# Kernel optimization log

Hardware: AMD Instinct MI355X
Metric: run time of the kernel (lower is better)

The kernel has to match this reference:

```python
import jax, jax.numpy as jnp
import numpy as np

IN_F, OUT_F = 512, 512
GRID_SIZE, SPLINE_ORDER = 5, 3
K = GRID_SIZE + SPLINE_ORDER  # 8 basis functions
B, S = 8, 1024


def setup_inputs() -> dict:
    key = jax.random.key(0)
    k1, k2, k3, k4, k5 = jax.random.split(key, 5)
    return {
        "x": jax.random.normal(k1, (B, S, IN_F), dtype=jnp.float32),
        "coeff": jax.random.normal(k2, (OUT_F, IN_F, K), dtype=jnp.float32),
        "scale_base": jax.random.normal(k3, (OUT_F, IN_F), dtype=jnp.float32) * 0.1,
        "scale_spline": jax.random.normal(k4, (OUT_F, IN_F), dtype=jnp.float32),
        "base_bias": jax.random.normal(k5, (OUT_F, IN_F), dtype=jnp.float32),
    }


def reference(x, coeff, scale_base, scale_spline, base_bias):
    batch = x.shape[0]
    in_f = x.shape[-1]
    k = coeff.shape[-1]

    xc = jnp.clip(x.reshape(-1, in_f), -1.0, 1.0)      # (N, in)
    base = jax.nn.silu(xc)                              # (N, in)

    # polynomial basis recurrence: b0 = 1, b1 = x, b_i = 2*x*b_{i-1} - 1
    bases = [jnp.ones_like(xc), xc]
    for _ in range(2, k):
        bases.append(2.0 * xc * bases[-1] - 1.0)
    basis = jnp.stack(bases[:k], axis=-1)               # (N, in, K)

    # spline[n,o] = sum_{i,k} scale_spline[o,i]*coeff[o,i,k]*basis[n,i,k]
    w_spline = scale_spline[..., None] * coeff          # (out, in, K)
    spline_term = jnp.einsum('nik,oik->no', basis, w_spline)
    base_term = base @ scale_base.T                     # (N, out)
    out = base_term + spline_term + jnp.sum(base_bias, axis=1)  # (N, out)

    out = out.reshape(batch, -1, base_bias.shape[0])    # (B, S, out)
    if out.shape[-2] == 1:
        out = out[..., 0, :]
    return out
```

## Files before the change

kernel.cpp:

```cpp
#include <hip/hip_runtime.h>
#include <hip/hip_bf16.h>

#define IN_FEAT 512
#define OUT_FEAT 512
#define NTOK 8192
#define KDIM 4096

typedef short bf16x8 __attribute__((ext_vector_type(8)));
typedef float f32x16 __attribute__((ext_vector_type(16)));

static __device__ inline short f2bf(float f) {
    union { float f; unsigned u; } v; v.f = f;
    unsigned u = v.u;
    u += 0x7fffu + ((u >> 16) & 1u);
    return (short)(u >> 16);
}

static __device__ inline unsigned pack2bf(float f0, float f1) {
    union { float f; unsigned u; } a, b; a.f = f0; b.f = f1;
    return __builtin_amdgcn_perm(b.u + 0x8000u, a.u + 0x8000u, 0x07060302u);
}

static __device__ inline bf16x8 gen_chunk(float xv) {
    float xc = fminf(fmaxf(xv, -1.f), 1.f);
    float e  = __expf(-xc);
    float bse = xc * __builtin_amdgcn_rcpf(1.f + e);
    float b2 = 2.f * xc * xc - 1.f;
    float b3 = 2.f * xc * b2 - 1.f;
    float b4 = 2.f * xc * b3 - 1.f;
    float b5 = 2.f * xc * b4 - 1.f;
    float b6 = 2.f * xc * b5 - 1.f;
    float b7 = 2.f * xc * b6 - 1.f;
    union { uint4 u; bf16x8 v; } r;
    r.u.x = pack2bf(bse, xc);
    r.u.y = pack2bf(b2, b3);
    r.u.z = pack2bf(b4, b5);
    r.u.w = pack2bf(b6, b7);
    return r.v;
}

static __device__ inline void gload_lds16(const short* g, short* l) {
    __builtin_amdgcn_global_load_lds(
        (const __attribute__((address_space(1))) unsigned int*)g,
        (__attribute__((address_space(3))) unsigned int*)l,
        16, 0, 0);
}

__global__ __launch_bounds__(256) void kan_prep(
    const float* __restrict__ coeff, const float* __restrict__ scale_base,
    const float* __restrict__ scale_spline, const float* __restrict__ base_bias,
    short* __restrict__ Wb, float* __restrict__ bias)
{
    int o = blockIdx.x;
    int tid = threadIdx.x;
    float local = 0.f;
#pragma unroll
    for (int rep = 0; rep < 2; ++rep) {
        int i = tid + rep * 256;
        size_t oi = (size_t)o * IN_FEAT + i;
        const float4* c4 = (const float4*)(coeff + oi * 8);
        float4 ca = c4[0], cb = c4[1];
        float ss = scale_spline[oi];
        float sb = scale_base[oi];
        local += base_bias[oi] + ss * ca.x;
        bf16x8 w;
        w[0] = f2bf(sb);
        w[1] = f2bf(ss * ca.y); w[2] = f2bf(ss * ca.z); w[3] = f2bf(ss * ca.w);
        w[4] = f2bf(ss * cb.x); w[5] = f2bf(ss * cb.y); w[6] = f2bf(ss * cb.z);
        w[7] = f2bf(ss * cb.w);
        *(bf16x8*)(Wb + (size_t)o * KDIM + (size_t)i * 8) = w;
    }
    __shared__ float red[4];
    for (int off = 32; off > 0; off >>= 1) local += __shfl_down(local, off, 64);
    int lane = tid & 63, wv = tid >> 6;
    if (lane == 0) red[wv] = local;
    __syncthreads();
    if (tid == 0) bias[o] = red[0] + red[1] + red[2] + red[3];
}

#define RSTR 67

__global__ __launch_bounds__(256, 4) void kan_gemm11(
    const float* __restrict__ x, const short* __restrict__ Wb,
    const float* __restrict__ bias, float* __restrict__ out)
{
    __shared__ __align__(16) short POOL[18432];
    short* Bs  = POOL;
    float* xsl = (float*)(POOL + 16384);

    int tid = threadIdx.x;
    int nb = blockIdx.x & 3;
    int mb = blockIdx.x >> 2;
    int m0 = mb * 64, o0 = nb * 128;

    int lane = tid & 63, wv = tid >> 6;
    int wn = wv & 1, kk = wv >> 1;
    int l31 = lane & 31, half = lane >> 5;

    f32x16 acc[2][2];
#pragma unroll
    for (int a = 0; a < 2; ++a)
#pragma unroll
        for (int b = 0; b < 2; ++b) acc[a][b] = (f32x16)0.f;

    int rg = lane >> 3;
    int g  = (lane & 7) ^ rg;
    const short* Bg = Wb + (size_t)(o0 + wv * 32 + rg) * KDIM
                         + (g >> 2) * 2048 + (g & 3) * 8;

    int xrow = tid >> 2, p = tid & 3;
    int xh = p >> 1, xq = p & 1;
    const float* xg = x + (size_t)(m0 + xrow) * IN_FEAT + xh * 256 + xq * 2;
    int sb0 = (xh * 4 + xq * 2) * 64 + xrow;

#define STAGE(buf, it)                                                        \
    {                                                                         \
        short* bd_ = Bs + (buf) * 8192 + wv * 2048;                           \
        const short* bg_ = Bg + (size_t)(it) * 32;                            \
        _Pragma("unroll")                                                     \
        for (int j = 0; j < 4; ++j)                                           \
            gload_lds16(bg_ + (size_t)j * 8 * KDIM, bd_ + j * 512);           \
        float2 v_ = *(const float2*)(xg + (size_t)(it) * 4);                  \
        float* xd_ = xsl + (buf) * 512 + sb0;                                 \
        xd_[0]  = v_.x;                                                       \
        xd_[64] = v_.y;                                                       \
    }

    STAGE(0, 0);
    int cur = 0;
    for (int it = 0; it < 64; ++it, cur ^= 1) {
        __syncthreads();
        if (it < 63) { int nxt = cur ^ 1; STAGE(nxt, it + 1); }
        const short* Bsc = Bs + cur * 8192;
        const float* xc_ = xsl + cur * 512;
#pragma unroll
        for (int istep = 0; istep < 2; ++istep) {
            int clog = kk * 4 + istep * 2 + half;
            bf16x8 bfr[2], af[2];
#pragma unroll
            for (int fn = 0; fn < 2; ++fn) {
                int row = wn * 64 + fn * 32 + l31;
                bfr[fn] = *(const bf16x8*)(Bsc + row * 64 + ((clog ^ (row & 7)) * 8));
            }
#pragma unroll
            for (int fm = 0; fm < 2; ++fm)
                af[fm] = gen_chunk(xc_[clog * 64 + fm * 32 + l31]);
#pragma unroll
            for (int fm = 0; fm < 2; ++fm)
#pragma unroll
                for (int fn = 0; fn < 2; ++fn)
                    acc[fm][fn] = __builtin_amdgcn_mfma_f32_32x32x16_bf16(
                        af[fm], bfr[fn], acc[fm][fn], 0, 0, 0);
        }
    }
#undef STAGE

    float* rbuf = (float*)POOL;
    int base = (wn * 64 + lane) * RSTR;
    __syncthreads();
    if (kk == 1) {
#pragma unroll
        for (int fm = 0; fm < 2; ++fm)
#pragma unroll
            for (int fn = 0; fn < 2; ++fn)
#pragma unroll
                for (int r = 0; r < 16; ++r)
                    rbuf[base + (fm * 2 + fn) * 16 + r] = acc[fm][fn][r];
    }
    __syncthreads();
    if (kk == 0) {
#pragma unroll
        for (int fn = 0; fn < 2; ++fn) {
            int o = o0 + wn * 64 + fn * 32 + l31;
            float bv = bias[o];
#pragma unroll
            for (int fm = 0; fm < 2; ++fm) {
#pragma unroll
                for (int r = 0; r < 16; ++r) {
                    float v = acc[fm][fn][r] + rbuf[base + (fm * 2 + fn) * 16 + r] + bv;
                    int token = m0 + fm * 32 + (r & 3) + 8 * (r >> 2) + 4 * half;
                    out[(size_t)token * OUT_FEAT + o] = v;
                }
            }
        }
    }
}

extern "C" void kernel_launch(void* const* d_in, const int* in_sizes, int n_in,
                              void* d_out, int out_size, void* d_ws, size_t ws_size,
                              hipStream_t stream) {
    const float* x            = (const float*)d_in[0];
    const float* coeff        = (const float*)d_in[1];
    const float* scale_base   = (const float*)d_in[2];
    const float* scale_spline = (const float*)d_in[3];
    const float* base_bias    = (const float*)d_in[4];
    float* out = (float*)d_out;

    short* Wb   = (short*)d_ws;
    float* bias = (float*)((char*)d_ws + (size_t)OUT_FEAT * KDIM * 2);

    kan_prep<<<OUT_FEAT, 256, 0, stream>>>(coeff, scale_base, scale_spline, base_bias, Wb, bias);
    kan_gemm11<<<(NTOK / 64) * (OUT_FEAT / 128), 256, 0, stream>>>(x, Wb, bias, out);
}
```

Before: 143.1 us.

## Shrink GEMM output tile to 64x64 and deepen K step per iteration

The output tile per block drops from 64x128 to 64x64, doubling the grid, and each loop iteration now covers 64 K-columns instead of 32, halving the iteration count. Warps now split along M rather than N, so each warp builds one A fragment per step and runs two MFMAs, with the two K-halves still reduced through LDS. The intent is more blocks for occupancy and load balance and fewer syncs per unit of K. The cost is that each wave recomputes basis expansions of x for twice as many output columns, and the weight tile reuse per loaded x drops.

```diff
diff --git a/kernel.cpp b/kernel.cpp
--- a/kernel.cpp
+++ b/kernel.cpp
@@ -78,109 +78,99 @@
     if (tid == 0) bias[o] = red[0] + red[1] + red[2] + red[3];
 }
 
-#define RSTR 67
+#define RSTR 33
 
-__global__ __launch_bounds__(256, 4) void kan_gemm11(
+__global__ __launch_bounds__(256, 4) void kan_gemm12(
     const float* __restrict__ x, const short* __restrict__ Wb,
     const float* __restrict__ bias, float* __restrict__ out)
 {
-    __shared__ __align__(16) short POOL[18432];
+    __shared__ __align__(16) short POOL[20480];
     short* Bs  = POOL;
     float* xsl = (float*)(POOL + 16384);
 
     int tid = threadIdx.x;
-    int nb = blockIdx.x & 3;
-    int mb = blockIdx.x >> 2;
-    int m0 = mb * 64, o0 = nb * 128;
+    int nb = blockIdx.x & 7;
+    int mb = blockIdx.x >> 3;
+    int m0 = mb * 64, o0 = nb * 64;
 
     int lane = tid & 63, wv = tid >> 6;
-    int wn = wv & 1, kk = wv >> 1;
+    int wm = wv & 1, kk = wv >> 1;
     int l31 = lane & 31, half = lane >> 5;
 
-    f32x16 acc[2][2];
-#pragma unroll
-    for (int a = 0; a < 2; ++a)
-#pragma unroll
-        for (int b = 0; b < 2; ++b) acc[a][b] = (f32x16)0.f;
+    f32x16 acc[2];
+    acc[0] = (f32x16)0.f; acc[1] = (f32x16)0.f;
 
     int rg = lane >> 3;
     int g  = (lane & 7) ^ rg;
-    const short* Bg = Wb + (size_t)(o0 + wv * 32 + rg) * KDIM
-                         + (g >> 2) * 2048 + (g & 3) * 8;
+    int kh = wv >> 1, rb = (wv & 1) * 32;
+    const short* Bg = Wb + (size_t)(o0 + rb + rg) * KDIM + kh * 2048 + g * 8;
+    int bdst0 = kh * 4096 + rb * 64;
 
     int xrow = tid >> 2, p = tid & 3;
-    int xh = p >> 1, xq = p & 1;
-    const float* xg = x + (size_t)(m0 + xrow) * IN_FEAT + xh * 256 + xq * 2;
-    int sb0 = (xh * 4 + xq * 2) * 64 + xrow;
+    const float* xg = x + (size_t)(m0 + xrow) * IN_FEAT + (p >> 1) * 256 + (p & 1) * 4;
+    int sb0 = (p * 4) * 64 + xrow;
 
 #define STAGE(buf, it)                                                        \
     {                                                                         \
-        short* bd_ = Bs + (buf) * 8192 + wv * 2048;                           \
-        const short* bg_ = Bg + (size_t)(it) * 32;                            \
+        short* bd_ = Bs + (buf) * 8192 + bdst0;                               \
+        const short* bg_ = Bg + (size_t)(it) * 64;                            \
         _Pragma("unroll")                                                     \
         for (int j = 0; j < 4; ++j)                                           \
             gload_lds16(bg_ + (size_t)j * 8 * KDIM, bd_ + j * 512);           \
-        float2 v_ = *(const float2*)(xg + (size_t)(it) * 4);                  \
-        float* xd_ = xsl + (buf) * 512 + sb0;                                 \
-        xd_[0]  = v_.x;                                                       \
-        xd_[64] = v_.y;                                                       \
+        float4 v_ = *(const float4*)(xg + (size_t)(it) * 8);                  \
+        float* xd_ = xsl + (buf) * 1024 + sb0;                                \
+        xd_[0]   = v_.x;                                                      \
+        xd_[64]  = v_.y;                                                      \
+        xd_[128] = v_.z;                                                      \
+        xd_[192] = v_.w;                                                      \
     }
 
     STAGE(0, 0);
     int cur = 0;
-    for (int it = 0; it < 64; ++it, cur ^= 1) {
+    for (int it = 0; it < 32; ++it, cur ^= 1) {
         __syncthreads();
-        if (it < 63) { int nxt = cur ^ 1; STAGE(nxt, it + 1); }
-        const short* Bsc = Bs + cur * 8192;
-        const float* xc_ = xsl + cur * 512;
+        if (it < 31) { int nxt = cur ^ 1; STAGE(nxt, it + 1); }
+        const short* Bsc = Bs + cur * 8192 + kk * 4096;
+        const float* xc_ = xsl + cur * 1024;
 #pragma unroll
-        for (int istep = 0; istep < 2; ++istep) {
-            int clog = kk * 4 + istep * 2 + half;
-            bf16x8 bfr[2], af[2];
+        for (int istep = 0; istep < 4; ++istep) {
+            int clog = istep * 2 + half;
+            bf16x8 bfr[2], af;
 #pragma unroll
             for (int fn = 0; fn < 2; ++fn) {
-                int row = wn * 64 + fn * 32 + l31;
+                int row = fn * 32 + l31;
                 bfr[fn] = *(const bf16x8*)(Bsc + row * 64 + ((clog ^ (row & 7)) * 8));
             }
+            af = gen_chunk(xc_[(kk * 8 + istep * 2 + half) * 64 + wm * 32 + l31]);
 #pragma unroll
-            for (int fm = 0; fm < 2; ++fm)
-                af[fm] = gen_chunk(xc_[clog * 64 + fm * 32 + l31]);
-#pragma unroll
-            for (int fm = 0; fm < 2; ++fm)
-#pragma unroll
-                for (int fn = 0; fn < 2; ++fn)
-                    acc[fm][fn] = __builtin_amdgcn_mfma_f32_32x32x16_bf16(
-                        af[fm], bfr[fn], acc[fm][fn], 0, 0, 0);
+            for (int fn = 0; fn < 2; ++fn)
+                acc[fn] = __builtin_amdgcn_mfma_f32_32x32x16_bf16(
+                    af, bfr[fn], acc[fn], 0, 0, 0);
         }
     }
 #undef STAGE
 
     float* rbuf = (float*)POOL;
-    int base = (wn * 64 + lane) * RSTR;
+    int base = (wm * 64 + lane) * RSTR;
     __syncthreads();
     if (kk == 1) {
 #pragma unroll
-        for (int fm = 0; fm < 2; ++fm)
+        for (int fn = 0; fn < 2; ++fn)
 #pragma unroll
-            for (int fn = 0; fn < 2; ++fn)
-#pragma unroll
-                for (int r = 0; r < 16; ++r)
-                    rbuf[base + (fm * 2 + fn) * 16 + r] = acc[fm][fn][r];
+            for (int r = 0; r < 16; ++r)
+                rbuf[base + fn * 16 + r] = acc[fn][r];
     }
     __syncthreads();
     if (kk == 0) {
 #pragma unroll
         for (int fn = 0; fn < 2; ++fn) {
-            int o = o0 + wn * 64 + fn * 32 + l31;
+            int o = o0 + fn * 32 + l31;
             float bv = bias[o];
 #pragma unroll
-            for (int fm = 0; fm < 2; ++fm) {
-#pragma unroll
-                for (int r = 0; r < 16; ++r) {
-                    float v = acc[fm][fn][r] + rbuf[base + (fm * 2 + fn) * 16 + r] + bv;
-                    int token = m0 + fm * 32 + (r & 3) + 8 * (r >> 2) + 4 * half;
-                    out[(size_t)token * OUT_FEAT + o] = v;
-                }
+            for (int r = 0; r < 16; ++r) {
+                float v = acc[fn][r] + rbuf[base + fn * 16 + r] + bv;
+                int token = m0 + wm * 32 + (r & 3) + 8 * (r >> 2) + 4 * half;
+                out[(size_t)token * OUT_FEAT + o] = v;
             }
         }
     }
@@ -200,5 +190,5 @@
     float* bias = (float*)((char*)d_ws + (size_t)OUT_FEAT * KDIM * 2);
 
     kan_prep<<<OUT_FEAT, 256, 0, stream>>>(coeff, scale_base, scale_spline, base_bias, Wb, bias);
-    kan_gemm11<<<(NTOK / 64) * (OUT_FEAT / 128), 256, 0, stream>>>(x, Wb, bias, out);
+    kan_gemm12<<<(NTOK / 64) * (OUT_FEAT / 64), 256, 0, stream>>>(x, Wb, bias, out);
 }
```

Result: faster. 139.0 us (-2.9%).

## Shrink output tile to 64x64 with four-way split-K across waves

Applied to the files above, without the earlier changes.

The GEMM tile changes from 64 tokens x 128 outputs to 64x64, which doubles the block count. Each of the four waves now takes a different K slice (split-K by 4) instead of a 2x2 N/K split. The K step per stage doubles to 128 and the swizzled LDS layouts change to match, and a two-stage LDS tree reduction combines the wave partials. The goal is more parallelism and fewer barriers, at the cost of recomputing the basis expansion for twice as many blocks and a heavier reduction epilogue.

```diff
diff --git a/kernel.cpp b/kernel.cpp
--- a/kernel.cpp
+++ b/kernel.cpp
@@ -78,24 +78,24 @@
     if (tid == 0) bias[o] = red[0] + red[1] + red[2] + red[3];
 }
 
-#define RSTR 67
-
-__global__ __launch_bounds__(256, 4) void kan_gemm11(
+__global__ __launch_bounds__(256, 4) void kan_gemm13(
     const float* __restrict__ x, const short* __restrict__ Wb,
     const float* __restrict__ bias, float* __restrict__ out)
 {
-    __shared__ __align__(16) short POOL[18432];
+    __shared__ __align__(16) short POOL[20480];
     short* Bs  = POOL;
     float* xsl = (float*)(POOL + 16384);
 
     int tid = threadIdx.x;
-    int nb = blockIdx.x & 3;
-    int mb = blockIdx.x >> 2;
-    int m0 = mb * 64, o0 = nb * 128;
+    int nb = blockIdx.x & 7;
+    int mb = blockIdx.x >> 3;
+    int m0 = mb * 64, o0 = nb * 64;
 
     int lane = tid & 63, wv = tid >> 6;
-    int wn = wv & 1, kk = wv >> 1;
+    int kk = wv;
     int l31 = lane & 31, half = lane >> 5;
+    int rm  = l31 & 15;
+    int xr0 = l31 ^ (kk * 8);
 
     f32x16 acc[2][2];
 #pragma unroll
@@ -103,81 +103,100 @@
 #pragma unroll
         for (int b = 0; b < 2; ++b) acc[a][b] = (f32x16)0.f;
 
-    int rg = lane >> 3;
-    int g  = (lane & 7) ^ rg;
-    const short* Bg = Wb + (size_t)(o0 + wv * 32 + rg) * KDIM
-                         + (g >> 2) * 2048 + (g & 3) * 8;
+    int rl = lane >> 4, q = lane & 15;
+    const short* pB0 = Wb + (size_t)(o0 + wv * 16 +  0 + rl) * KDIM + (size_t)(q ^ ( 0 + rl)) * 8;
+    const short* pB1 = Wb + (size_t)(o0 + wv * 16 +  4 + rl) * KDIM + (size_t)(q ^ ( 4 + rl)) * 8;
+    const short* pB2 = Wb + (size_t)(o0 + wv * 16 +  8 + rl) * KDIM + (size_t)(q ^ ( 8 + rl)) * 8;
+    const short* pB3 = Wb + (size_t)(o0 + wv * 16 + 12 + rl) * KDIM + (size_t)(q ^ (12 + rl)) * 8;
 
     int xrow = tid >> 2, p = tid & 3;
-    int xh = p >> 1, xq = p & 1;
-    const float* xg = x + (size_t)(m0 + xrow) * IN_FEAT + xh * 256 + xq * 2;
-    int sb0 = (xh * 4 + xq * 2) * 64 + xrow;
+    const float* xg = x + (size_t)(m0 + xrow) * IN_FEAT + p * 4;
+    int xb = p * 256 + (xrow ^ (p * 8));
 
 #define STAGE(buf, it)                                                        \
     {                                                                         \
         short* bd_ = Bs + (buf) * 8192 + wv * 2048;                           \
-        const short* bg_ = Bg + (size_t)(it) * 32;                            \
-        _Pragma("unroll")                                                     \
-        for (int j = 0; j < 4; ++j)                                           \
-            gload_lds16(bg_ + (size_t)j * 8 * KDIM, bd_ + j * 512);           \
-        float2 v_ = *(const float2*)(xg + (size_t)(it) * 4);                  \
-        float* xd_ = xsl + (buf) * 512 + sb0;                                 \
-        xd_[0]  = v_.x;                                                       \
-        xd_[64] = v_.y;                                                       \
+        gload_lds16(pB0 + (size_t)(it) * 128, bd_);                           \
+        gload_lds16(pB1 + (size_t)(it) * 128, bd_ + 512);                     \
+        gload_lds16(pB2 + (size_t)(it) * 128, bd_ + 1024);                    \
+        gload_lds16(pB3 + (size_t)(it) * 128, bd_ + 1536);                    \
+        float4 v_ = *(const float4*)(xg + (size_t)(it) * 16);                 \
+        float* xd_ = xsl + (buf) * 1024 + xb;                                 \
+        xd_[0]   = v_.x;                                                      \
+        xd_[64]  = v_.y;                                                      \
+        xd_[128] = v_.z;                                                      \
+        xd_[192] = v_.w;                                                      \
     }
 
     STAGE(0, 0);
     int cur = 0;
-    for (int it = 0; it < 64; ++it, cur ^= 1) {
+    for (int it = 0; it < 32; ++it, cur ^= 1) {
         __syncthreads();
-        if (it < 63) { int nxt = cur ^ 1; STAGE(nxt, it + 1); }
+        if (it < 31) { int nxt = cur ^ 1; STAGE(nxt, it + 1); }
         const short* Bsc = Bs + cur * 8192;
-        const float* xc_ = xsl + cur * 512;
+        const float* xc_ = xsl + cur * 1024;
 #pragma unroll
         for (int istep = 0; istep < 2; ++istep) {
-            int clog = kk * 4 + istep * 2 + half;
-            bf16x8 bfr[2], af[2];
-#pragma unroll
-            for (int fn = 0; fn < 2; ++fn) {
-                int row = wn * 64 + fn * 32 + l31;
-                bfr[fn] = *(const bf16x8*)(Bsc + row * 64 + ((clog ^ (row & 7)) * 8));
-            }
-#pragma unroll
-            for (int fm = 0; fm < 2; ++fm)
-                af[fm] = gen_chunk(xc_[clog * 64 + fm * 32 + l31]);
-#pragma unroll
-            for (int fm = 0; fm < 2; ++fm)
-#pragma unroll
-                for (int fn = 0; fn < 2; ++fn)
-                    acc[fm][fn] = __builtin_amdgcn_mfma_f32_32x32x16_bf16(
-                        af[fm], bfr[fn], acc[fm][fn], 0, 0, 0);
+            int s = kk * 4 + istep * 2 + half;
+            bf16x8 af0 = gen_chunk(xc_[s * 64 + xr0]);
+            bf16x8 af1 = gen_chunk(xc_[s * 64 + 32 + xr0]);
+            int ph = (s ^ rm) * 8;
+            bf16x8 b0 = *(const bf16x8*)(Bsc + l31 * 128 + ph);
+            bf16x8 b1 = *(const bf16x8*)(Bsc + (32 + l31) * 128 + ph);
+            acc[0][0] = __builtin_amdgcn_mfma_f32_32x32x16_bf16(af0, b0, acc[0][0], 0, 0, 0);
+            acc[0][1] = __builtin_amdgcn_mfma_f32_32x32x16_bf16(af0, b1, acc[0][1], 0, 0, 0);
+            acc[1][0] = __builtin_amdgcn_mfma_f32_32x32x16_bf16(af1, b0, acc[1][0], 0, 0, 0);
+            acc[1][1] = __builtin_amdgcn_mfma_f32_32x32x16_bf16(af1, b1, acc[1][1], 0, 0, 0);
         }
     }
 #undef STAGE
 
     float* rbuf = (float*)POOL;
-    int base = (wn * 64 + lane) * RSTR;
+    __syncthreads();
+    if (kk >= 2) {
+        float* s_ = rbuf + (size_t)(kk - 2) * 4224 + lane * 66;
+#pragma unroll
+        for (int fm = 0; fm < 2; ++fm)
+#pragma unroll
+            for (int fn = 0; fn < 2; ++fn)
+#pragma unroll
+                for (int r = 0; r < 16; ++r)
+                    s_[(fm * 2 + fn) * 16 + r] = acc[fm][fn][r];
+    }
+    __syncthreads();
+    if (kk < 2) {
+        const float* s_ = rbuf + (size_t)kk * 4224 + lane * 66;
+#pragma unroll
+        for (int fm = 0; fm < 2; ++fm)
+#pragma unroll
+            for (int fn = 0; fn < 2; ++fn)
+#pragma unroll
+                for (int r = 0; r < 16; ++r)
+                    acc[fm][fn][r] += s_[(fm * 2 + fn) * 16 + r];
+    }
     __syncthreads();
     if (kk == 1) {
+        float* s_ = rbuf + lane * 66;
 #pragma unroll
         for (int fm = 0; fm < 2; ++fm)
 #pragma unroll
             for (int fn = 0; fn < 2; ++fn)
 #pragma unroll
                 for (int r = 0; r < 16; ++r)
-                    rbuf[base + (fm * 2 + fn) * 16 + r] = acc[fm][fn][r];
+                    s_[(fm * 2 + fn) * 16 + r] = acc[fm][fn][r];
     }
     __syncthreads();
     if (kk == 0) {
+        const float* s_ = rbuf + lane * 66;
 #pragma unroll
         for (int fn = 0; fn < 2; ++fn) {
-            int o = o0 + wn * 64 + fn * 32 + l31;
+            int o = o0 + fn * 32 + l31;
             float bv = bias[o];
 #pragma unroll
             for (int fm = 0; fm < 2; ++fm) {
 #pragma unroll
                 for (int r = 0; r < 16; ++r) {
-                    float v = acc[fm][fn][r] + rbuf[base + (fm * 2 + fn) * 16 + r] + bv;
+                    float v = acc[fm][fn][r] + s_[(fm * 2 + fn) * 16 + r] + bv;
                     int token = m0 + fm * 32 + (r & 3) + 8 * (r >> 2) + 4 * half;
                     out[(size_t)token * OUT_FEAT + o] = v;
                 }
@@ -200,5 +219,5 @@
     float* bias = (float*)((char*)d_ws + (size_t)OUT_FEAT * KDIM * 2);
 
     kan_prep<<<OUT_FEAT, 256, 0, stream>>>(coeff, scale_base, scale_spline, base_bias, Wb, bias);
-    kan_gemm11<<<(NTOK / 64) * (OUT_FEAT / 128), 256, 0, stream>>>(x, Wb, bias, out);
-}
+    kan_gemm13<<<(NTOK / 64) * (OUT_FEAT / 64), 256, 0, stream>>>(x, Wb, bias, out);
+}
```

Result: faster. 137.7 us (-3.8%).
